# Kernel tuning notes

Hardware: AMD Instinct MI355X
Metric: run time of the kernel (lower is better)

## Reference

```python
import jax, jax.numpy as jnp
import numpy as np

L, T, B, D, H, DQK, DV, FF = 4, 1024, 4, 1024, 16, 64, 64, 4096
EPS = 1e-6


def setup_inputs() -> dict:
    key = jax.random.key(0)
    ks = jax.random.split(key, 11)
    s = 0.02
    f32 = jnp.float32
    return {
        "x": jax.random.normal(ks[0], (T, B, D), f32),
        "mask": jnp.ones((B, T), bool),
        "Wk": jax.random.normal(ks[1], (L, D, H * DQK), f32) * s,
        "bk": jnp.zeros((L, H * DQK), f32),
        "Wq": jax.random.normal(ks[2], (L, D, H * DQK), f32) * s,
        "bq": jnp.zeros((L, H * DQK), f32),
        "Wv": jax.random.normal(ks[3], (L, D, H * DV), f32) * s,
        "bv": jnp.zeros((L, H * DV), f32),
        "W1": jax.random.normal(ks[4], (L, D, FF), f32) * s,
        "b1": jnp.zeros((L, FF), f32),
        "W2": jax.random.normal(ks[5], (L, FF, D), f32) * s,
        "b2": jnp.zeros((L, D), f32),
    }


def _resnorm(x, fx):
    # residual + (x - mean) / (std + eps); torch.std is unbiased (ddof=1)
    y = x + fx
    mu = y.mean(-1, keepdims=True)
    sd = y.std(-1, keepdims=True, ddof=1)
    return (y - mu) / (sd + EPS)


def _ff(x, W1, b1, W2, b2):
    # Feedforward default puts ReLU after every linear layer, including the last
    h = jax.nn.relu(x @ W1 + b1)
    return jax.nn.relu(h @ W2 + b2)


def _attn(x, mask, Wk, bk, Wq, bq, Wv, bv):
    # x: (T, B, D); mask: (B, T)
    k = (x @ Wk + bk).reshape(T, B, H, DQK)
    q = (x @ Wq + bq).reshape(T, B, H, DQK)
    # kern[b,h,i,j] = <key_i, query_j> / sqrt(D)   (note: scaled by model dim D)
    kern = jnp.einsum('ibhj,kbhj->bhik', k, q) / np.sqrt(D)
    kern = jnp.where(mask[:, None, None, :], kern, -jnp.inf)
    A = jax.nn.softmax(kern, axis=-1)  # softmax over query axis (as in source)
    v = (x @ Wv + bv).reshape(T, B, H, DV)
    out = jnp.einsum('bhij,jbhk->ibhk', A, v)  # (T, B, H, DV)
    return out.reshape(T, B, H * DV)


def reference(x, mask, Wk, bk, Wq, bq, Wv, bv, W1, b1, W2, b2):
    for l in range(L):
        z = _resnorm(x, _ff(x, W1[l], b1[l], W2[l], b2[l]))
        x = _resnorm(z, _attn(z, mask, Wk[l], bk[l], Wq[l], bq[l], Wv[l], bv[l]))
    return x
```

## Files before the change

### kernel.cpp

```cpp
#include <hip/hip_runtime.h>
#include <cstdint>
#include <cstddef>

#define TT    1024
#define DD    1024
#define FFD   4096
#define NLAYER 4
#define MROWS 4096

typedef __bf16 bf16;
typedef __bf16 bf16x8 __attribute__((ext_vector_type(8)));
typedef __bf16 bf16x4v __attribute__((ext_vector_type(4)));
typedef float  f32x4  __attribute__((ext_vector_type(4)));

__device__ __forceinline__ bf16 f2b(float f) { return (bf16)f; }

typedef __attribute__((address_space(3))) unsigned int lds_u32;
typedef __attribute__((address_space(1))) const unsigned int g_u32;
__device__ __forceinline__ void gl_lds16(const bf16* g, bf16* l) {
    __builtin_amdgcn_global_load_lds((g_u32*)g, (lds_u32*)l, 16, 0, 0);
}

template <int N> __device__ __forceinline__ void waitcnt_vm() {
    if constexpr (N == 0)      asm volatile("s_waitcnt vmcnt(0)" ::: "memory");
    else if constexpr (N == 3) asm volatile("s_waitcnt vmcnt(3)" ::: "memory");
    else if constexpr (N == 6) asm volatile("s_waitcnt vmcnt(6)" ::: "memory");
    else if constexpr (N == 8) asm volatile("s_waitcnt vmcnt(8)" ::: "memory");
    else static_assert(N == 0, "unsupported vmcnt literal");
}

__global__ __launch_bounds__(256) void cvt_k(const float* __restrict__ src,
                                             bf16* __restrict__ dst) {
    const int i = blockIdx.x * 256 + threadIdx.x;
    f32x4 v = *(const f32x4*)(src + (size_t)i * 4);
    bf16x4v o;
#pragma unroll
    for (int u = 0; u < 4; ++u) o[u] = f2b(v[u]);
    *(bf16x4v*)(dst + (size_t)i * 4) = o;
}

__device__ __forceinline__ void tr_tile(const float* __restrict__ src,
                                        bf16* __restrict__ dst, int R, int C,
                                        int bx, int by, int t) {
    __shared__ bf16 tile[32][33];
    const int tx = t & 31, ty = (t >> 5) * 4;
    const int c0 = bx * 32, r0 = by * 32;
#pragma unroll
    for (int u = 0; u < 4; ++u)
        tile[ty + u][tx] = f2b(src[(size_t)(r0 + ty + u) * C + c0 + tx]);
    __syncthreads();
#pragma unroll
    for (int u = 0; u < 4; ++u)
        dst[(size_t)(c0 + ty + u) * R + r0 + tx] = tile[tx][ty + u];
}

__global__ __launch_bounds__(256) void prep_k(const float* __restrict__ W1,
                                              const float* __restrict__ W2,
                                              const float* __restrict__ Wk,
                                              const float* __restrict__ Wq,
                                              const float* __restrict__ Wv,
                                              const float* __restrict__ bkp,
                                              const float* __restrict__ bqp,
                                              const float* __restrict__ bvp,
                                              bf16* __restrict__ w1t,
                                              bf16* __restrict__ w2t,
                                              bf16* __restrict__ kqvt,
                                              float* __restrict__ bcat) {
    const int id = blockIdx.x, t = threadIdx.x;
    if (id < 4096) {
        tr_tile(W1, w1t, 1024, 4096, id & 127, id >> 7, t);
    } else if (id < 8192) {
        const int r = id - 4096;
        tr_tile(W2, w2t, 4096, 1024, r & 31, r >> 5, t);
    } else if (id < 9216) {
        const int r = id - 8192;
        tr_tile(Wk, kqvt, 1024, 1024, r & 31, r >> 5, t);
    } else if (id < 10240) {
        const int r = id - 9216;
        tr_tile(Wq, kqvt + 1048576, 1024, 1024, r & 31, r >> 5, t);
    } else if (id < 11264) {
        const int r = id - 10240;
        tr_tile(Wv, kqvt + 2097152, 1024, 1024, r & 31, r >> 5, t);
    } else {
        const int i = (id - 11264) * 256 + t;
        bcat[i] = (i < 1024) ? bkp[i] : (i < 2048 ? bqp[i - 1024] : bvp[i - 2048]);
    }
}

__global__ __launch_bounds__(256) void vtrans_k(const bf16* __restrict__ src,
                                                bf16* __restrict__ dst) {
    __shared__ bf16 tile[32][33];
    const int t  = threadIdx.x;
    const int tx = t & 31, ty = (t >> 5) * 4;
    const int bh = blockIdx.z, tt = blockIdx.y * 32, dv0 = blockIdx.x * 32;
    const int b = bh >> 4, h = bh & 15;
#pragma unroll
    for (int u = 0; u < 4; ++u)
        tile[ty + u][tx] = src[(size_t)((tt + ty + u) * 4 + b) * 3072 + h * 64 + dv0 + tx];
    __syncthreads();
#pragma unroll
    for (int u = 0; u < 4; ++u)
        dst[(size_t)(bh * 64 + dv0 + ty + u) * 1024 + tt + tx] = tile[tx][ty + u];
}

template <bool RELU, int BN, int NBUF, int NWAVE>
__global__ __launch_bounds__(NWAVE * 64) void gemm_bt(const bf16* __restrict__ A, int lda,
                                                      const bf16* __restrict__ Bt, int ldb,
                                                      const float* __restrict__ bias,
                                                      bf16* __restrict__ C, int ldc, int K) {
    static_assert(NBUF == 1 || (NBUF == 2 && BN == 64 && NWAVE == 8), "cfg");
    constexpr int WC = (BN == 128) ? 2 : (NWAVE == 8 ? 2 : 1);
    constexpr int MW = 128 / (NWAVE / WC);
    constexpr int NW = BN / WC;
    constexpr int MI = MW / 16;
    constexpr int NI = NW / 16;
    constexpr int AG = 16 / NWAVE;
    constexpr int BG = (BN / 8) / NWAVE;
    constexpr int LPS = AG + BG;
    __shared__ bf16 As[NBUF][128 * 64];
    __shared__ bf16 Bs[NBUF][BN * 64];
    const int t = threadIdx.x;
    const int w = t >> 6, lane = t & 63, l15 = lane & 15, qd = lane >> 4;
    int bid = blockIdx.y * gridDim.x + blockIdx.x;
    {
        const int q = (int)(gridDim.x * gridDim.y) >> 3;
        bid = (bid & 7) * q + (bid >> 3);
    }
    const int bx = bid % (int)gridDim.x, by = bid / (int)gridDim.x;
    const int m0 = by * 128, n0 = bx * BN;
    const int wr = (w / WC) * MW, wc = (w % WC) * NW;
    const int srow = lane >> 3, scol = ((lane & 7) ^ srow) * 8;
    const int sx = (l15 & 7) << 3;
    f32x4 acc[MI][NI] = {};

    auto stage = [&](int buf, int k0) {
#pragma unroll
        for (int i = 0; i < AG; ++i) {
            const int r0 = (w * AG + i) * 8;
            gl_lds16(A + (size_t)(m0 + r0 + srow) * lda + k0 + scol,
                     &As[buf][0] + r0 * 64 + lane * 8);
        }
#pragma unroll
        for (int i = 0; i < BG; ++i) {
            const int r0 = (w * BG + i) * 8;
            gl_lds16(Bt + (size_t)(n0 + r0 + srow) * ldb + k0 + scol,
                     &Bs[buf][0] + r0 * 64 + lane * 8);
        }
    };
    auto compute = [&](int buf) {
#pragma unroll
        for (int kk = 0; kk < 64; kk += 32) {
            bf16x8 af[MI], bfr[NI];
#pragma unroll
            for (int i = 0; i < MI; ++i)
                af[i] = *(const bf16x8*)(&As[buf][0] + (wr + i * 16 + l15) * 64 + ((kk + qd * 8) ^ sx));
#pragma unroll
            for (int j = 0; j < NI; ++j)
                bfr[j] = *(const bf16x8*)(&Bs[buf][0] + (wc + j * 16 + l15) * 64 + ((kk + qd * 8) ^ sx));
#pragma unroll
            for (int i = 0; i < MI; ++i)
#pragma unroll
                for (int j = 0; j < NI; ++j)
                    acc[i][j] = __builtin_amdgcn_mfma_f32_16x16x32_bf16(af[i], bfr[j], acc[i][j], 0, 0, 0);
        }
    };

    if (NBUF == 2) {
        const int nt = K >> 6;
        stage(0, 0);
        for (int it = 0; it < nt; ++it) {
            if (it + 1 < nt) {
                stage((it + 1) & 1, (it + 1) << 6);
                waitcnt_vm<LPS>();
            } else {
                waitcnt_vm<0>();
            }
            __builtin_amdgcn_s_barrier();
            compute(it & 1);
            __builtin_amdgcn_s_barrier();
        }
    } else {
        for (int k0 = 0; k0 < K; k0 += 64) {
            stage(0, k0);
            __syncthreads();
            compute(0);
            __syncthreads();
        }
    }

#pragma unroll
    for (int j = 0; j < NI; ++j) {
        const int col = n0 + wc + j * 16 + l15;
        const float bz = bias[col];
#pragma unroll
        for (int i = 0; i < MI; ++i) {
            const int row = m0 + wr + i * 16 + qd * 4;
#pragma unroll
            for (int p = 0; p < 4; ++p) {
                float c = acc[i][j][p] + bz;
                if (RELU) c = fmaxf(c, 0.f);
                C[(size_t)(row + p) * ldc + col] = f2b(c);
            }
        }
    }
}

__device__ __forceinline__ float block_sum(float s, float* red, int w, int lane) {
#pragma unroll
    for (int off = 32; off >= 1; off >>= 1) s += __shfl_xor(s, off, 64);
    if (lane == 0) red[w] = s;
    __syncthreads();
    return red[0] + red[1] + red[2] + red[3];
}

template <bool OUT_F32>
__global__ __launch_bounds__(256) void resnorm_k(const bf16* __restrict__ x,
                                                 const bf16* __restrict__ fx,
                                                 void* __restrict__ outv) {
    __shared__ float red1[4], red2[4];
    const int t = threadIdx.x, w = t >> 6, lane = t & 63;
    const size_t base = (size_t)blockIdx.x * DD + t * 4;
    bf16x4v xv = *(const bf16x4v*)(x + base);
    bf16x4v fv = *(const bf16x4v*)(fx + base);
    float y[4], s = 0.f;
#pragma unroll
    for (int u = 0; u < 4; ++u) { y[u] = (float)xv[u] + (float)fv[u]; s += y[u]; }
    s = block_sum(s, red1, w, lane);
    const float mu = s * (1.f / DD);
    float v = 0.f;
#pragma unroll
    for (int u = 0; u < 4; ++u) { const float d = y[u] - mu; v += d * d; }
    v = block_sum(v, red2, w, lane);
    const float sd = sqrtf(v * (1.f / (DD - 1)));
    const float ri = 1.f / (sd + 1e-6f);
    if (OUT_F32) {
        f32x4 ov;
#pragma unroll
        for (int u = 0; u < 4; ++u) ov[u] = (y[u] - mu) * ri;
        *(f32x4*)((float*)outv + base) = ov;
    } else {
        bf16x4v ov;
#pragma unroll
        for (int u = 0; u < 4; ++u) ov[u] = f2b((y[u] - mu) * ri);
        *(bf16x4v*)((bf16*)outv + base) = ov;
    }
}

__global__ __launch_bounds__(256, 2) void attn_k(const bf16* __restrict__ kq,
                                                 const bf16* __restrict__ vt,
                                                 bf16* __restrict__ out) {
    __shared__ bf16 smem[17408 + 9216 + 8704];
    bf16* PlK = smem;
    bf16* Qt  = smem + 17408;
    bf16* Vts = smem + 17408 + 9216;
    const int t = threadIdx.x;
    const int w = t >> 6, lane = t & 63, l15 = lane & 15, qd = lane >> 4;
    int bid = blockIdx.y * 8 + blockIdx.x;
    bid = (bid & 7) * 64 + (bid >> 3);
    const int i0 = (bid & 7) * 128, bh = bid >> 3, b = bh >> 4, h = bh & 15;
    const size_t kbase = (size_t)b * 3072 + h * 64;
    const int sr = t >> 3, sc = (t & 7) * 8;
    const int vr = t >> 2, vc = (t & 3) * 32;
    const float SC = 0.03125f;

#pragma unroll
    for (int ch = 0; ch < 4; ++ch) {
        const int r = ch * 32 + sr;
        *(bf16x8*)(PlK + r * 72 + sc) =
            *(const bf16x8*)(kq + (size_t)(i0 + r) * 12288 + kbase + sc);
    }
    __syncthreads();
    bf16x8 kf[2][2];
#pragma unroll
    for (int i = 0; i < 2; ++i)
#pragma unroll
        for (int kx = 0; kx < 2; ++kx)
            kf[i][kx] = *(const bf16x8*)(PlK + (w * 32 + i * 16 + l15) * 72 + kx * 32 + qd * 8);
    bf16* Pl = PlK + w * 4352;

    f32x4 acc_o[2][4] = {};
    float lsum[2][4] = {};

    for (int j0 = 0; j0 < TT; j0 += 128) {
#pragma unroll
        for (int ch = 0; ch < 4; ++ch) {
            const int r = ch * 32 + sr;
            *(bf16x8*)(Qt + r * 72 + sc) =
                *(const bf16x8*)(kq + (size_t)(j0 + r) * 12288 + kbase + 1024 + sc);
        }
#pragma unroll
        for (int u = 0; u < 4; ++u)
            *(bf16x8*)(Vts + vr * 136 + vc + u * 8) =
                *(const bf16x8*)(vt + (size_t)(bh * 64 + vr) * 1024 + j0 + vc + u * 8);
        __syncthreads();

        f32x4 accs[2][8] = {};
#pragma unroll
        for (int kx = 0; kx < 2; ++kx) {
            bf16x8 bfr[8];
#pragma unroll
            for (int j = 0; j < 8; ++j)
                bfr[j] = *(const bf16x8*)(Qt + (j * 16 + l15) * 72 + kx * 32 + qd * 8);
#pragma unroll
            for (int i = 0; i < 2; ++i)
#pragma unroll
                for (int j = 0; j < 8; ++j)
                    accs[i][j] = __builtin_amdgcn_mfma_f32_16x16x32_bf16(kf[i][kx], bfr[j], accs[i][j], 0, 0, 0);
        }

#pragma unroll
        for (int i = 0; i < 2; ++i)
#pragma unroll
            for (int j = 0; j < 8; ++j)
#pragma unroll
                for (int p = 0; p < 4; ++p) {
                    const float pv = __expf(accs[i][j][p] * SC);
                    lsum[i][p] += pv;
                    Pl[(i * 16 + qd * 4 + p) * 136 + j * 16 + l15] = f2b(pv);
                }

#pragma unroll
        for (int kt = 0; kt < 4; ++kt) {
            bf16x8 pa[2], vb[4];
#pragma unroll
            for (int i = 0; i < 2; ++i)
                pa[i] = *(const bf16x8*)(Pl + (i * 16 + l15) * 136 + kt * 32 + qd * 8);
#pragma unroll
            for (int n = 0; n < 4; ++n)
                vb[n] = *(const bf16x8*)(Vts + (n * 16 + l15) * 136 + kt * 32 + qd * 8);
#pragma unroll
            for (int i = 0; i < 2; ++i)
#pragma unroll
                for (int n = 0; n < 4; ++n)
                    acc_o[i][n] = __builtin_amdgcn_mfma_f32_16x16x32_bf16(pa[i], vb[n], acc_o[i][n], 0, 0, 0);
        }
        __syncthreads();
    }

#pragma unroll
    for (int i = 0; i < 2; ++i)
#pragma unroll
        for (int p = 0; p < 4; ++p) {
            float s = lsum[i][p];
#pragma unroll
            for (int off = 1; off < 16; off <<= 1) s += __shfl_xor(s, off, 64);
            const float ri = 1.f / s;
            const int ig = i0 + w * 32 + i * 16 + qd * 4 + p;
#pragma unroll
            for (int n = 0; n < 4; ++n)
                out[(size_t)ig * 4096 + b * 1024 + h * 64 + n * 16 + l15] = f2b(acc_o[i][n][p] * ri);
        }
}

extern "C" void kernel_launch(void* const* d_in, const int* in_sizes, int n_in,
                              void* d_out, int out_size, void* d_ws, size_t ws_size,
                              hipStream_t stream) {
    const float* x_in = (const float*)d_in[0];
    const float* Wk = (const float*)d_in[2];
    const float* bk = (const float*)d_in[3];
    const float* Wq = (const float*)d_in[4];
    const float* bq = (const float*)d_in[5];
    const float* Wv = (const float*)d_in[6];
    const float* bv = (const float*)d_in[7];
    const float* W1 = (const float*)d_in[8];
    const float* b1 = (const float*)d_in[9];
    const float* W2 = (const float*)d_in[10];
    const float* b2 = (const float*)d_in[11];

    bf16* ws = (bf16*)d_ws;
    const size_t M1 = 1024 * 1024;
    bf16* w1t  = ws;
    bf16* w2t  = ws +  4 * M1;
    bf16* kqvt = ws +  8 * M1;
    bf16* vtb  = ws + 11 * M1;
    bf16* fbuf = ws + 15 * M1;
    bf16* zbuf = ws + 19 * M1;
    bf16* xb   = ws + 23 * M1;
    bf16* big  = ws + 27 * M1;
    float* bcat = (float*)(ws + 43 * M1);
    float* outp = (float*)d_out;

    cvt_k<<<dim3(MROWS * DD / 1024), 256, 0, stream>>>(x_in, xb);

    const bf16* xcur = xb;
    for (int l = 0; l < NLAYER; ++l) {
        prep_k<<<dim3(11276), 256, 0, stream>>>(
            W1 + (size_t)l * DD * FFD, W2 + (size_t)l * FFD * DD,
            Wk + (size_t)l * M1, Wq + (size_t)l * M1, Wv + (size_t)l * M1,
            bk + (size_t)l * DD, bq + (size_t)l * DD, bv + (size_t)l * DD,
            w1t, w2t, kqvt, bcat);
        gemm_bt<true, 128, 1, 4><<<dim3(FFD / 128, MROWS / 128), 256, 0, stream>>>(
            xcur, DD, w1t, DD, b1 + (size_t)l * FFD, big, FFD, DD);
        gemm_bt<true, 64, 2, 8><<<dim3(DD / 64, MROWS / 128), 512, 0, stream>>>(
            big, FFD, w2t, FFD, b2 + (size_t)l * DD, fbuf, DD, FFD);
        resnorm_k<false><<<dim3(MROWS), 256, 0, stream>>>(xcur, fbuf, zbuf);
        gemm_bt<false, 128, 1, 4><<<dim3(3072 / 128, MROWS / 128), 256, 0, stream>>>(
            zbuf, DD, kqvt, DD, bcat, big, 3072, DD);
        vtrans_k<<<dim3(2, 32, 64), 256, 0, stream>>>(big + 2048, vtb);
        attn_k<<<dim3(8, 64), 256, 0, stream>>>(big, vtb, fbuf);
        if (l == NLAYER - 1)
            resnorm_k<true><<<dim3(MROWS), 256, 0, stream>>>(zbuf, fbuf, outp);
        else
            resnorm_k<false><<<dim3(MROWS), 256, 0, stream>>>(zbuf, fbuf, xb);
        xcur = xb;
    }
}
```

Baseline: 1.017 ms.

## Use 256x256 double-buffered 8-wave GEMM for the first FFN layer

Adds a new GEMM kernel with 256x256 output tiles, 8 waves, double-buffered direct global-to-LDS loads, XOR-swizzled LDS reads, interleaved quadrant MFMA scheduling with priority bumps, and a block-index remap for L2 locality. It replaces the 128x128 single-buffer GEMM used for the x@W1 FFN projection. The aim is more data reuse per tile and overlap of loads with MFMAs. The trade-off is a grid of only 256 blocks with 128 KB of LDS each, so occupancy drops and a 256-CU device may be underfilled.

```diff
diff --git a/kernel.cpp b/kernel.cpp
--- a/kernel.cpp
+++ b/kernel.cpp
@@ -103,6 +103,105 @@
         dst[(size_t)(bh * 64 + dv0 + ty + u) * 1024 + tt + tx] = tile[tx][ty + u];
 }
 
+template <bool RELU>
+__global__ __launch_bounds__(512) void gemm256(const bf16* __restrict__ A, int lda,
+                                               const bf16* __restrict__ Bt, int ldb,
+                                               const float* __restrict__ bias,
+                                               bf16* __restrict__ C, int ldc, int K) {
+    __shared__ bf16 As[2][256 * 64];
+    __shared__ bf16 Bs[2][256 * 64];
+    const int t = threadIdx.x;
+    const int w = t >> 6, lane = t & 63, l15 = lane & 15, qd = lane >> 4;
+    int bid = blockIdx.y * gridDim.x + blockIdx.x;
+    {
+        const int q = (int)(gridDim.x * gridDim.y) >> 3;
+        bid = (bid & 7) * q + (bid >> 3);
+    }
+    const int bx = bid % (int)gridDim.x, by = bid / (int)gridDim.x;
+    const int m0 = by * 256, n0 = bx * 256;
+    const int wr = (w >> 2) * 128;
+    const int wc = (w & 3) * 64;
+    const int srow = lane >> 3, scol = ((lane & 7) ^ srow) * 8;
+    const int sx = (l15 & 7) << 3;
+    f32x4 acc[8][4] = {};
+    bf16x8 af[4][2], bfr[4][2];
+
+    auto stage = [&](int buf, int k0) {
+#pragma unroll
+        for (int i = 0; i < 4; ++i) {
+            const int r0 = (w * 4 + i) * 8;
+            gl_lds16(A + (size_t)(m0 + r0 + srow) * lda + k0 + scol,
+                     &As[buf][0] + r0 * 64 + lane * 8);
+            gl_lds16(Bt + (size_t)(n0 + r0 + srow) * ldb + k0 + scol,
+                     &Bs[buf][0] + r0 * 64 + lane * 8);
+        }
+    };
+    auto rdA = [&](int ih, int b) {
+#pragma unroll
+        for (int i = 0; i < 4; ++i)
+#pragma unroll
+            for (int kx = 0; kx < 2; ++kx)
+                af[i][kx] = *(const bf16x8*)(&As[b][0] + (wr + (ih * 4 + i) * 16 + l15) * 64
+                                             + ((kx * 32 + qd * 8) ^ sx));
+    };
+    auto rdB = [&](int jh, int b) {
+#pragma unroll
+        for (int j = 0; j < 2; ++j)
+#pragma unroll
+            for (int kx = 0; kx < 2; ++kx)
+                bfr[jh * 2 + j][kx] = *(const bf16x8*)(&Bs[b][0] + (wc + (jh * 2 + j) * 16 + l15) * 64
+                                                       + ((kx * 32 + qd * 8) ^ sx));
+    };
+    auto mfmaQ = [&](int ih, int jh) {
+        __builtin_amdgcn_s_setprio(1);
+#pragma unroll
+        for (int kx = 0; kx < 2; ++kx)
+#pragma unroll
+            for (int i = 0; i < 4; ++i)
+#pragma unroll
+                for (int j = 0; j < 2; ++j)
+                    acc[ih * 4 + i][jh * 2 + j] = __builtin_amdgcn_mfma_f32_16x16x32_bf16(
+                        af[i][kx], bfr[jh * 2 + j][kx], acc[ih * 4 + i][jh * 2 + j], 0, 0, 0);
+        __builtin_amdgcn_s_setprio(0);
+    };
+
+    const int nt = K >> 6;
+    stage(0, 0);
+    for (int g = 0; g < nt; ++g) {
+        const int b = g & 1;
+        waitcnt_vm<0>();
+        __builtin_amdgcn_s_barrier();
+        if (g + 1 < nt) stage(b ^ 1, (g + 1) << 6);
+        rdA(0, b); rdB(0, b);
+        __builtin_amdgcn_s_barrier();
+        mfmaQ(0, 0);
+        rdB(1, b);
+        __builtin_amdgcn_s_barrier();
+        mfmaQ(0, 1);
+        rdA(1, b);
+        __builtin_amdgcn_s_barrier();
+        mfmaQ(1, 1);
+        __builtin_amdgcn_s_barrier();
+        mfmaQ(1, 0);
+    }
+
+#pragma unroll
+    for (int j = 0; j < 4; ++j) {
+        const int col = n0 + wc + j * 16 + l15;
+        const float bz = bias[col];
+#pragma unroll
+        for (int i = 0; i < 8; ++i) {
+            const int row = m0 + wr + i * 16 + qd * 4;
+#pragma unroll
+            for (int p = 0; p < 4; ++p) {
+                float c = acc[i][j][p] + bz;
+                if (RELU) c = fmaxf(c, 0.f);
+                C[(size_t)(row + p) * ldc + col] = f2b(c);
+            }
+        }
+    }
+}
+
 template <bool RELU, int BN, int NBUF, int NWAVE>
 __global__ __launch_bounds__(NWAVE * 64) void gemm_bt(const bf16* __restrict__ A, int lda,
                                                       const bf16* __restrict__ Bt, int ldb,
@@ -389,7 +488,7 @@
             Wk + (size_t)l * M1, Wq + (size_t)l * M1, Wv + (size_t)l * M1,
             bk + (size_t)l * DD, bq + (size_t)l * DD, bv + (size_t)l * DD,
             w1t, w2t, kqvt, bcat);
-        gemm_bt<true, 128, 1, 4><<<dim3(FFD / 128, MROWS / 128), 256, 0, stream>>>(
+        gemm256<true><<<dim3(FFD / 256, MROWS / 256), 512, 0, stream>>>(
             xcur, DD, w1t, DD, b1 + (size_t)l * FFD, big, FFD, DD);
         gemm_bt<true, 64, 2, 8><<<dim3(DD / 64, MROWS / 128), 512, 0, stream>>>(
             big, FFD, w2t, FFD, b2 + (size_t)l * DD, fbuf, DD, FFD);
```

New measurement: 981.4 us. 1.04x faster.
